# Optimization experiments

Hardware: AMD Instinct MI355X
Metric: run time of the kernel (lower is better)

Reference implementation:

```python
import jax, jax.numpy as jnp
import numpy as np

B, S, W = 32, 128, 20
WV, CV = 50000, 128
WD, CE = 300, 50
KS = (2, 3, 4, 5)
NF = 64
TOTF = NF * len(KS)
CF = 300
H = 512
L = 9
LP = L + 2
START, END = L, L + 1
NEG = -10000.0


def setup_inputs():
    key = jax.random.key(0)
    ks = jax.random.split(key, 40)
    def nrm(i, shape, scale=0.1):
        return jax.random.normal(ks[i], shape, dtype=jnp.float32) * scale
    inp = {}
    inp['token_ids'] = jax.random.randint(ks[0], (B, S), 0, WV)
    inp['char_ids'] = jax.random.randint(ks[1], (B, S, W), 0, CV)
    lens = jnp.sort(jax.random.randint(ks[2], (B,), S // 2, S + 1))[::-1]
    inp['lens'] = lens.astype(jnp.int32)
    inp['labels'] = jax.random.randint(ks[3], (B, S), 0, L)
    inp['word_embed'] = nrm(4, (WV, WD))
    inp['char_embed'] = nrm(5, (CV, CE))
    for j, k in enumerate(KS):
        inp['conv_w%d' % k] = nrm(6 + j, (k, CE, NF))
        inp['conv_b%d' % k] = nrm(10 + j, (NF,))
    inp['ff_w'] = nrm(14, (CF, TOTF))
    inp['ff_b'] = nrm(15, (CF,))
    inp['wgate_w'] = nrm(16, (WD, WD))
    inp['cgate_w'] = nrm(17, (CF, CF))
    inp['gate_w'] = nrm(18, (WD, WD))
    inp['wih_f'] = nrm(19, (4 * H, WD))
    inp['whh_f'] = nrm(20, (4 * H, H))
    inp['b_f'] = nrm(21, (4 * H,))
    inp['wih_b'] = nrm(22, (4 * H, WD))
    inp['whh_b'] = nrm(23, (4 * H, H))
    inp['b_b'] = nrm(24, (4 * H,))
    inp['out_w'] = nrm(25, (L, 2 * H))
    inp['out_b'] = nrm(26, (L,))
    inp['trn'] = nrm(27, (LP, LP))
    return inp


def _char_cnn(char_ids, char_embed, convs):
    x = char_embed[char_ids.reshape(-1, W)]  # [B*S, W, CE]
    feats = []
    for w, b in convs:
        y = jax.lax.conv_general_dilated(x, w, (1,), 'VALID',
                                         dimension_numbers=('NWC', 'WIO', 'NWC')) + b
        feats.append(jnp.max(jax.nn.relu(y), axis=1))  # max over time -> [B*S, NF]
    return jnp.concatenate(feats, axis=1)  # [B*S, TOTF]


def _run_lstm(x, mask, wih, whh, b, reverse):
    # x [B,S,D], mask bool [B,S]; padded steps freeze state and emit zeros (packed-seq semantics)
    xg = jnp.einsum('bsd,gd->bsg', x, wih) + b  # [B,S,4H]
    xg_t = jnp.swapaxes(xg, 0, 1)               # [S,B,4H]
    m_t = jnp.swapaxes(mask, 0, 1)[..., None]   # [S,B,1]
    h0 = jnp.zeros((x.shape[0], H), x.dtype)
    def step(carry, inp):
        h, c = carry
        g_t, m = inp
        g = g_t + h @ whh.T
        i, f, gg, o = jnp.split(g, 4, axis=-1)  # torch gate order i,f,g,o
        cn = jax.nn.sigmoid(f) * c + jax.nn.sigmoid(i) * jnp.tanh(gg)
        hn = jax.nn.sigmoid(o) * jnp.tanh(cn)
        h = jnp.where(m, hn, h)
        c = jnp.where(m, cn, c)
        return (h, c), jnp.where(m, hn, 0.0)
    _, out = jax.lax.scan(step, (h0, h0), (xg_t, m_t), reverse=reverse)
    return jnp.swapaxes(out, 0, 1)  # [B,S,H]


def _crf_norm(logits, mask, trn):
    # logits [B,S,LP]; trn[i,j] = score(prev=j -> next=i)
    alpha = logits[:, 0] + trn[:, START][None, :]
    lt = jnp.swapaxes(logits, 0, 1)[1:]                 # [S-1,B,LP]
    mt = jnp.swapaxes(mask, 0, 1)[1:][..., None]        # [S-1,B,1]
    def step(alpha, inp):
        lg, m = inp
        new = jax.scipy.special.logsumexp(alpha[:, None, :] + trn[None], axis=2) + lg
        return jnp.where(m, new, alpha), None
    alpha, _ = jax.lax.scan(step, alpha, (lt, mt))
    return jax.scipy.special.logsumexp(alpha + trn[END][None, :], axis=1)


def _crf_gold(logits, labels, lens, mask, trn):
    fm = mask.astype(logits.dtype)
    emit = jnp.take_along_axis(logits, labels[..., None], axis=2)[..., 0]
    emit = jnp.sum(emit * fm, axis=1)
    trans = trn[labels[:, 1:], labels[:, :-1]] * fm[:, 1:]
    first = trn[labels[:, 0], START]
    last_lab = jnp.take_along_axis(labels, (lens - 1)[:, None], axis=1)[:, 0]
    return emit + jnp.sum(trans, axis=1) + first + trn[END, last_lab]


def reference(token_ids, char_ids, lens, labels, word_embed, char_embed,
              conv_w2, conv_b2, conv_w3, conv_b3, conv_w4, conv_b4, conv_w5, conv_b5,
              ff_w, ff_b, wgate_w, cgate_w, gate_w,
              wih_f, whh_f, b_f, wih_b, whh_b, b_b, out_w, out_b, trn):
    word_in = word_embed[token_ids]                               # [B,S,WD]
    convs = [(conv_w2, conv_b2), (conv_w3, conv_b3), (conv_w4, conv_b4), (conv_w5, conv_b5)]
    ch = _char_cnn(char_ids, char_embed, convs)                   # [B*S,TOTF]
    char_in = (ch @ ff_w.T + ff_b).reshape(B, S, CF)              # CharCNNFF output
    g = jax.nn.sigmoid(jnp.tanh(word_in @ wgate_w.T + char_in @ cgate_w.T) @ gate_w.T)
    feats = g * word_in + (1.0 - g) * char_in                     # gated fusion (dropout = eval identity)
    mask = jnp.arange(S)[None, :] < lens[:, None]                 # [B,S] bool
    hf = _run_lstm(feats, mask, wih_f, whh_f, b_f, False)
    hb = _run_lstm(feats, mask, wih_b, whh_b, b_b, True)
    lstm_out = jnp.concatenate([hf, hb], axis=-1)                 # [B,S,2H]
    logits = lstm_out @ out_w.T + out_b                           # [B,S,L]
    pads = jnp.full((B, S, 2), NEG, logits.dtype)
    logits = jnp.concatenate([logits, pads], axis=2)              # pad_logits -> [B,S,LP]
    norm = _crf_norm(logits, mask, trn)
    gold = _crf_gold(logits, labels, lens, mask, trn)
    loglik = gold - norm
    return (loglik, logits)
```

## Files before the change

kernel.cpp:

```cpp
#include <hip/hip_runtime.h>

#define NB    32
#define SEQ   128
#define WCH   20
#define CED   50
#define NFLT  64
#define WDIM  300
#define HD    512
#define NWORD 4096
#define LPAD  11
#define NEGV  -10000.0f
#define LSTM_BLOCKS 16

typedef float f32x4 __attribute__((ext_vector_type(4)));
typedef float f32x16 __attribute__((ext_vector_type(16)));
typedef __bf16 bf16x8 __attribute__((ext_vector_type(8)));
typedef unsigned short u16x8 __attribute__((ext_vector_type(8)));
typedef unsigned short u16x4 __attribute__((ext_vector_type(4)));
typedef unsigned long long ull;

static __device__ __forceinline__ unsigned short f2bf(float f) {
  unsigned u = __builtin_bit_cast(unsigned, f);
  u += 0x7fffu + ((u >> 16) & 1u);
  return (unsigned short)(u >> 16);
}
static __device__ __forceinline__ float bf2f(unsigned short s) {
  unsigned u = ((unsigned)s) << 16;
  return __builtin_bit_cast(float, u);
}
static __device__ __forceinline__ float sigf(float x) { return 1.0f / (1.0f + expf(-x)); }

__global__ __launch_bounds__(256) void conv_kernel(
    const int* __restrict__ char_ids, const float* __restrict__ char_embed,
    const float* __restrict__ w2, const float* __restrict__ b2,
    const float* __restrict__ w3, const float* __restrict__ b3,
    const float* __restrict__ w4, const float* __restrict__ b4,
    const float* __restrict__ w5, const float* __restrict__ b5,
    float* __restrict__ ch)
{
  __shared__ __align__(16) float xT[CED][WCH];
  int wi = blockIdx.x;
  int tid = threadIdx.x;
  for (int e = tid; e < WCH * CED; e += 256) {
    int p = e / CED, c = e - p * CED;
    int cid = char_ids[wi * WCH + p];
    xT[c][p] = char_embed[cid * CED + c];
  }
  __syncthreads();
  int w = tid >> 6, f = tid & 63;
  int k = w + 2;
  int P = WCH - k + 1;
  const float* cw = (w == 0) ? w2 : (w == 1) ? w3 : (w == 2) ? w4 : w5;
  const float* cb = (w == 0) ? b2 : (w == 1) ? b3 : (w == 2) ? b4 : b5;
  float acc[19];
  #pragma unroll
  for (int p = 0; p < 19; p++) acc[p] = 0.f;
  for (int c = 0; c < CED; c++) {
    float xr[20];
    const float4* rowp = (const float4*)&xT[c][0];
    #pragma unroll
    for (int q = 0; q < 5; q++) {
      float4 v = rowp[q];
      xr[4*q+0] = v.x; xr[4*q+1] = v.y; xr[4*q+2] = v.z; xr[4*q+3] = v.w;
    }
    #pragma unroll
    for (int dw = 0; dw < 5; dw++) {
      if (dw < k) {
        float wv = cw[(dw * CED + c) * NFLT + f];
        #pragma unroll
        for (int p = 0; p < 19; p++) {
          if (p < P) acc[p] += xr[p + dw] * wv;
        }
      }
    }
  }
  float m = acc[0];
  #pragma unroll
  for (int p = 1; p < 19; p++) if (p < P) m = fmaxf(m, acc[p]);
  ch[wi * 256 + w * 64 + f] = fmaxf(0.f, m + cb[f]);
}

__global__ void gather_word_kernel(const int* __restrict__ token_ids,
                                   const float* __restrict__ word_embed,
                                   float* __restrict__ word_in)
{
  int idx = blockIdx.x * 256 + threadIdx.x;
  if (idx < NWORD * WDIM) {
    int i = idx / WDIM, c = idx - i * WDIM;
    word_in[idx] = word_embed[token_ids[i] * WDIM + c];
  }
}

__global__ __launch_bounds__(256) void gemm_bt_kernel(
    const float* __restrict__ A, const float* __restrict__ Bw,
    const float* __restrict__ bias, const float* __restrict__ Cin,
    float* __restrict__ Cout, unsigned short* __restrict__ Cbf,
    int M, int N, int K, int act, int gridN)
{
  __shared__ __align__(16) unsigned short As[128 * 32];
  __shared__ __align__(16) unsigned short Bs[128 * 32];
  int bid = blockIdx.x;
  int tm = bid / gridN, tn = bid - tm * gridN;
  int m0 = tm * 128, n0 = tn * 128;
  int tid = threadIdx.x;
  int lane = tid & 63, w = tid >> 6;
  int wr = (w >> 1) * 64, wc = (w & 1) * 64;
  f32x4 acc[4][4] = {};
  int fr = lane & 15, fk = (lane >> 4) * 8;

  for (int k0 = 0; k0 < K; k0 += 32) {
    __syncthreads();
    #pragma unroll
    for (int i = 0; i < 4; i++) {
      int idx = tid + i * 256;
      int r = idx >> 3, c4 = idx & 7;
      int kx = k0 + c4 * 4;
      int ra = m0 + r, rb = n0 + r;
      f32x4 av = {0.f,0.f,0.f,0.f}, bv = {0.f,0.f,0.f,0.f};
      if (kx < K) {
        if (ra < M) av = *(const f32x4*)&A[(size_t)ra * K + kx];
        if (rb < N) bv = *(const f32x4*)&Bw[(size_t)rb * K + kx];
      }
      u16x4 ap, bp;
      #pragma unroll
      for (int j = 0; j < 4; j++) { ap[j] = f2bf(av[j]); bp[j] = f2bf(bv[j]); }
      *(u16x4*)&As[r * 32 + c4 * 4] = ap;
      *(u16x4*)&Bs[r * 32 + c4 * 4] = bp;
    }
    __syncthreads();
    bf16x8 a[4], b[4];
    #pragma unroll
    for (int mt = 0; mt < 4; mt++)
      a[mt] = *(const bf16x8*)&As[(wr + mt * 16 + fr) * 32 + fk];
    #pragma unroll
    for (int nt = 0; nt < 4; nt++)
      b[nt] = *(const bf16x8*)&Bs[(wc + nt * 16 + fr) * 32 + fk];
    #pragma unroll
    for (int mt = 0; mt < 4; mt++)
      #pragma unroll
      for (int nt = 0; nt < 4; nt++)
        acc[mt][nt] = __builtin_amdgcn_mfma_f32_16x16x32_bf16(a[mt], b[nt], acc[mt][nt], 0, 0, 0);
  }

  #pragma unroll
  for (int mt = 0; mt < 4; mt++) {
    #pragma unroll
    for (int nt = 0; nt < 4; nt++) {
      #pragma unroll
      for (int j = 0; j < 4; j++) {
        int row = m0 + wr + mt * 16 + (lane >> 4) * 4 + j;
        int col = n0 + wc + nt * 16 + (lane & 15);
        if (row < M && col < N) {
          float v = acc[mt][nt][j];
          if (Cin)  v += Cin[(size_t)row * N + col];
          if (bias) v += bias[col];
          if (act == 1)      v = tanhf(v);
          else if (act == 2) v = sigf(v);
          if (Cbf) Cbf[(size_t)row * N + col] = f2bf(v);
          else     Cout[(size_t)row * N + col] = v;
        }
      }
    }
  }
}

__global__ void feats_kernel(const float* __restrict__ g, const float* __restrict__ word_in,
                             const float* __restrict__ char_in, float* __restrict__ feats,
                             unsigned* __restrict__ flags)
{
  if (blockIdx.x == 0 && threadIdx.x < 32)
    __hip_atomic_store(&flags[threadIdx.x], 0u, __ATOMIC_RELAXED, __HIP_MEMORY_SCOPE_AGENT);
  int idx = blockIdx.x * 256 + threadIdx.x;
  if (idx < NWORD * WDIM) {
    float gg = g[idx];
    feats[idx] = gg * word_in[idx] + (1.f - gg) * char_in[idx];
  }
}

__global__ __launch_bounds__(512, 2) void lstm_kernel(
    const unsigned short* __restrict__ xg_f, const unsigned short* __restrict__ xg_b,
    const float* __restrict__ whh_f, const float* __restrict__ whh_b,
    const int* __restrict__ lens,
    float* __restrict__ lstm_out, unsigned short* __restrict__ h_glob,
    unsigned* __restrict__ flags)
{
  int bid = blockIdx.x;
  int dir = bid >> 3, sl = bid & 7;
  int hs0 = sl << 6;
  int tid = threadIdx.x, lane = tid & 63, w = tid >> 6;
  int g = w & 3, hc = w >> 2;
  int l31 = lane & 31, le = lane >> 5;
  const unsigned short* xg = dir ? xg_b : xg_f;
  const float* whh = dir ? whh_b : whh_f;
  unsigned short* hg = h_glob + dir * (2 * NB * HD);
  unsigned* myflags = flags + dir * 16;

  bf16x8 wf[32];
  {
    const float* src = whh + (size_t)(g * HD + hs0 + hc * 32 + l31) * HD + le * 8;
    #pragma unroll
    for (int kk = 0; kk < 32; kk++) {
      u16x8 tv;
      #pragma unroll
      for (int j = 0; j < 8; j++) tv[j] = f2bf(src[kk * 16 + j]);
      wf[kk] = __builtin_bit_cast(bf16x8, tv);
    }
  }

  __shared__ __align__(16) unsigned short hS[16384];
  __shared__ float Gs[NB][260];

  int b = tid >> 4;
  int u = (tid & 15) << 2;
  int srow = tid >> 4, sq = tid & 15;
  int mylen = lens[b];
  float c4[4] = {0.f,0.f,0.f,0.f}, hp4[4] = {0.f,0.f,0.f,0.f};

  ull xq0, xq1, xq2, xq3;
  {
    int t0 = dir ? (SEQ - 1) : 0;
    const ull* xp = (const ull*)&xg[((size_t)(b * SEQ + t0)) * 2048 + hs0 + u];
    xq0 = xp[0]; xq1 = xp[128]; xq2 = xp[256]; xq3 = xp[384];
  }

  for (int s = 0; s < SEQ; s++) {
    int t = dir ? (SEQ - 1 - s) : s;
    f32x16 acc0 = {}, acc1 = {};

    if (s > 0) {
      if (w == 0) {
        unsigned tgt = (unsigned)s;
        for (;;) {
          unsigned v = (lane < 8)
            ? __hip_atomic_load(&myflags[lane], __ATOMIC_RELAXED, __HIP_MEMORY_SCOPE_AGENT)
            : tgt;
          if (__all(v >= tgt)) break;
          __builtin_amdgcn_s_sleep(1);
        }
      }
      __syncthreads();
      {
        const ull* hq = (const ull*)(hg + (s & 1) * (NB * HD));
        ull v[8];
        #pragma unroll
        for (int i = 0; i < 8; i++)
          v[i] = __hip_atomic_load(hq + srow * 128 + sq * 8 + i, __ATOMIC_RELAXED, __HIP_MEMORY_SCOPE_AGENT);
        int rs = ((srow ^ (sq & 7)) & 31) << 4;
        #pragma unroll
        for (int e2 = 0; e2 < 4; e2++) {
          int kk = 2 * sq + (e2 >> 1), e = e2 & 1;
          uint4 qv;
          qv.x = (unsigned)v[2*e2];     qv.y = (unsigned)(v[2*e2] >> 32);
          qv.z = (unsigned)v[2*e2+1];   qv.w = (unsigned)(v[2*e2+1] >> 32);
          *(uint4*)((char*)hS + (((kk * 2 + e) << 9) + rs)) = qv;
        }
      }
      __syncthreads();
      #pragma unroll
      for (int kk = 0; kk < 32; kk += 2) {
        int rs = ((l31 ^ ((kk >> 1) & 7)) & 31) << 4;
        int a0off = ((kk * 2 + le) << 9) + rs;
        int a1off = ((kk * 2 + 2 + le) << 9) + rs;
        bf16x8 a0 = *(const bf16x8*)((const char*)hS + a0off);
        bf16x8 a1 = *(const bf16x8*)((const char*)hS + a1off);
        acc0 = __builtin_amdgcn_mfma_f32_32x32x16_bf16(a0, wf[kk], acc0, 0, 0, 0);
        acc1 = __builtin_amdgcn_mfma_f32_32x32x16_bf16(a1, wf[kk+1], acc1, 0, 0, 0);
      }
    }

    #pragma unroll
    for (int r = 0; r < 16; r++) {
      int bb = (r & 3) + 8 * (r >> 2) + 4 * le;
      Gs[bb][g * 64 + hc * 32 + l31] = acc0[r] + acc1[r];
    }
    __syncthreads();

    f32x4 gi  = *(const f32x4*)&Gs[b][u];
    f32x4 gfv = *(const f32x4*)&Gs[b][64 + u];
    f32x4 ggv = *(const f32x4*)&Gs[b][128 + u];
    f32x4 gov = *(const f32x4*)&Gs[b][192 + u];
    bool mk = (t < mylen);
    f32x4 outv;
    ull hpk = 0;
    #pragma unroll
    for (int j = 0; j < 4; j++) {
      float xi = bf2f((unsigned short)(xq0 >> (16*j)));
      float xf = bf2f((unsigned short)(xq1 >> (16*j)));
      float xG = bf2f((unsigned short)(xq2 >> (16*j)));
      float xo = bf2f((unsigned short)(xq3 >> (16*j)));
      float iv = sigf(xi + gi[j]);
      float fv = sigf(xf + gfv[j]);
      float Gv = tanhf(xG + ggv[j]);
      float ov = sigf(xo + gov[j]);
      float cn = fv * c4[j] + iv * Gv;
      float hn = ov * tanhf(cn);
      if (mk) c4[j] = cn;
      float hk = mk ? hn : hp4[j];
      hp4[j] = hk;
      outv[j] = mk ? hn : 0.f;
      hpk |= ((ull)f2bf(hk)) << (16*j);
    }
    {
      ull* hd = (ull*)(hg + ((s & 1) ^ 1) * (NB * HD));
      __hip_atomic_store(&hd[(b * HD + hs0 + u) >> 2], hpk, __ATOMIC_RELAXED, __HIP_MEMORY_SCOPE_AGENT);
    }

    __syncthreads();
    if (tid == 0)
      __hip_atomic_store(&myflags[sl], (unsigned)(s + 1), __ATOMIC_RELAXED, __HIP_MEMORY_SCOPE_AGENT);

    size_t obase = ((size_t)(b * SEQ + t)) * 1024 + dir * HD + hs0 + u;
    *(f32x4*)&lstm_out[obase] = outv;
    if (s + 1 < SEQ) {
      int tn = dir ? (SEQ - 2 - s) : (s + 1);
      const ull* xp = (const ull*)&xg[((size_t)(b * SEQ + tn)) * 2048 + hs0 + u];
      xq0 = xp[0]; xq1 = xp[128]; xq2 = xp[256]; xq3 = xp[384];
    }
  }
}

__global__ __launch_bounds__(64) void logits_kernel(
    const float* __restrict__ lstm_out, const float* __restrict__ out_w,
    const float* __restrict__ out_b, float* __restrict__ lg)
{
  int rw = blockIdx.x, j = threadIdx.x;
  const float* row = lstm_out + (size_t)rw * 1024;
  float s[9];
  #pragma unroll
  for (int l = 0; l < 9; l++) s[l] = 0.f;
  for (int e = j; e < 1024; e += 64) {
    float x = row[e];
    #pragma unroll
    for (int l = 0; l < 9; l++) s[l] += x * out_w[l * 1024 + e];
  }
  #pragma unroll
  for (int l = 0; l < 9; l++) {
    #pragma unroll
    for (int off = 32; off > 0; off >>= 1) s[l] += __shfl_xor(s[l], off);
  }
  float v = NEGV;
  if (j < 9) {
    float r = (j==0)?s[0]:(j==1)?s[1]:(j==2)?s[2]:(j==3)?s[3]:(j==4)?s[4]:
              (j==5)?s[5]:(j==6)?s[6]:(j==7)?s[7]:s[8];
    v = r + out_b[j];
  }
  if (j < LPAD) lg[(size_t)rw * LPAD + j] = v;
}

__global__ __launch_bounds__(64) void crf_gold_kernel(
    const float* __restrict__ lg, const int* __restrict__ labels,
    const int* __restrict__ lens, const float* __restrict__ trn, float* __restrict__ gold)
{
  int b = blockIdx.x, j = threadIdx.x;
  int len = lens[b];
  const int* lab = labels + b * SEQ;
  const float* l0 = lg + (size_t)b * SEQ * LPAD;
  float s = 0.f;
  for (int t = j; t < SEQ; t += 64) {
    if (t < len) {
      s += l0[t * LPAD + lab[t]];
      if (t >= 1) s += trn[lab[t] * LPAD + lab[t - 1]];
    }
  }
  #pragma unroll
  for (int off = 32; off > 0; off >>= 1) s += __shfl_xor(s, off);
  if (j == 0) {
    s += trn[lab[0] * LPAD + 9];
    s += trn[10 * LPAD + lab[len - 1]];
    gold[b] = s;
  }
}

__global__ __launch_bounds__(64) void crf_norm_kernel(
    const float* __restrict__ lg, const int* __restrict__ lens,
    const float* __restrict__ trn, const float* __restrict__ gold, float* __restrict__ out_ll)
{
  int b = blockIdx.x, i = threadIdx.x;
  int len = lens[b];
  const float* l0 = lg + (size_t)b * SEQ * LPAD;
  bool act = (i < LPAD);
  float trow[LPAD];
  #pragma unroll
  for (int jj = 0; jj < LPAD; jj++) trow[jj] = act ? trn[i * LPAD + jj] : 0.f;
  float alpha = act ? (l0[i] + trow[9]) : -1e30f;

  for (int t = 1; t < SEQ; t++) {
    float vj[LPAD];
    #pragma unroll
    for (int jj = 0; jj < LPAD; jj++) vj[jj] = __shfl(alpha, jj) + trow[jj];
    float mx = vj[0];
    #pragma unroll
    for (int jj = 1; jj < LPAD; jj++) mx = fmaxf(mx, vj[jj]);
    float sum = 0.f;
    #pragma unroll
    for (int jj = 0; jj < LPAD; jj++) sum += expf(vj[jj] - mx);
    float lgv = act ? l0[t * LPAD + i] : 0.f;
    float nw = mx + logf(sum) + lgv;
    if (act && t < len) alpha = nw;
  }
  float vj[LPAD];
  #pragma unroll
  for (int jj = 0; jj < LPAD; jj++) vj[jj] = __shfl(alpha, jj) + trn[10 * LPAD + jj];
  float mx = vj[0];
  #pragma unroll
  for (int jj = 1; jj < LPAD; jj++) mx = fmaxf(mx, vj[jj]);
  float sum = 0.f;
  #pragma unroll
  for (int jj = 0; jj < LPAD; jj++) sum += expf(vj[jj] - mx);
  if (i == 0) out_ll[b] = gold[b] - (mx + logf(sum));
}

extern "C" void kernel_launch(void* const* d_in, const int* in_sizes, int n_in,
                              void* d_out, int out_size, void* d_ws, size_t ws_size,
                              hipStream_t stream)
{
  (void)in_sizes; (void)n_in; (void)out_size; (void)ws_size;
  const int*   token_ids = (const int*)d_in[0];
  const int*   char_ids  = (const int*)d_in[1];
  const int*   lens      = (const int*)d_in[2];
  const int*   labels    = (const int*)d_in[3];
  const float* word_embed= (const float*)d_in[4];
  const float* char_embed= (const float*)d_in[5];
  const float* w2 = (const float*)d_in[6];  const float* cb2 = (const float*)d_in[7];
  const float* w3 = (const float*)d_in[8];  const float* cb3 = (const float*)d_in[9];
  const float* w4 = (const float*)d_in[10]; const float* cb4 = (const float*)d_in[11];
  const float* w5 = (const float*)d_in[12]; const float* cb5 = (const float*)d_in[13];
  const float* ff_w = (const float*)d_in[14]; const float* ff_b = (const float*)d_in[15];
  const float* wgate_w = (const float*)d_in[16];
  const float* cgate_w = (const float*)d_in[17];
  const float* gate_w  = (const float*)d_in[18];
  const float* wih_f = (const float*)d_in[19]; const float* whh_f = (const float*)d_in[20];
  const float* b_f   = (const float*)d_in[21];
  const float* wih_b = (const float*)d_in[22]; const float* whh_b = (const float*)d_in[23];
  const float* b_b   = (const float*)d_in[24];
  const float* out_w = (const float*)d_in[25]; const float* out_b = (const float*)d_in[26];
  const float* trn   = (const float*)d_in[27];

  char* ws = (char*)d_ws;
  size_t off = 0;
  auto alloc = [&](size_t bytes) { void* p = ws + off; off += (bytes + 255) & ~(size_t)255; return p; };
  float* ch       = (float*)alloc((size_t)NWORD * 256 * 4);
  float* word_in  = (float*)alloc((size_t)NWORD * WDIM * 4);
  float* char_in  = (float*)alloc((size_t)NWORD * WDIM * 4);
  float* t1       = (float*)alloc((size_t)NWORD * WDIM * 4);
  float* gbuf     = (float*)alloc((size_t)NWORD * WDIM * 4);
  float* feats    = (float*)alloc((size_t)NWORD * WDIM * 4);
  unsigned short* xgf = (unsigned short*)alloc((size_t)NWORD * 2048 * 2);
  unsigned short* xgb = (unsigned short*)alloc((size_t)NWORD * 2048 * 2);
  float* lstm_o   = (float*)alloc((size_t)NWORD * 1024 * 4);
  unsigned short* hglob = (unsigned short*)alloc((size_t)2 * 2 * NB * HD * 2);
  float* gold     = (float*)alloc((size_t)NB * 4);
  unsigned* flags = (unsigned*)alloc(256);

  float* outp   = (float*)d_out;
  float* loglik = outp;
  float* logits = outp + NB;

  conv_kernel<<<NWORD, 256, 0, stream>>>(char_ids, char_embed, w2, cb2, w3, cb3, w4, cb4, w5, cb5, ch);
  gather_word_kernel<<<(NWORD * WDIM + 255) / 256, 256, 0, stream>>>(token_ids, word_embed, word_in);
  gemm_bt_kernel<<<32 * 3, 256, 0, stream>>>(ch, ff_w, ff_b, nullptr, char_in, nullptr, NWORD, 300, 256, 0, 3);
  gemm_bt_kernel<<<32 * 3, 256, 0, stream>>>(word_in, wgate_w, nullptr, nullptr, t1, nullptr, NWORD, 300, 300, 0, 3);
  gemm_bt_kernel<<<32 * 3, 256, 0, stream>>>(char_in, cgate_w, nullptr, t1, t1, nullptr, NWORD, 300, 300, 1, 3);
  gemm_bt_kernel<<<32 * 3, 256, 0, stream>>>(t1, gate_w, nullptr, nullptr, gbuf, nullptr, NWORD, 300, 300, 2, 3);
  feats_kernel<<<(NWORD * WDIM + 255) / 256, 256, 0, stream>>>(gbuf, word_in, char_in, feats, flags);
  gemm_bt_kernel<<<32 * 16, 256, 0, stream>>>(feats, wih_f, b_f, nullptr, nullptr, xgf, NWORD, 2048, 300, 0, 16);
  gemm_bt_kernel<<<32 * 16, 256, 0, stream>>>(feats, wih_b, b_b, nullptr, nullptr, xgb, NWORD, 2048, 300, 0, 16);
  {
    void* args[] = { (void*)&xgf, (void*)&xgb, (void*)&whh_f, (void*)&whh_b,
                     (void*)&lens, (void*)&lstm_o, (void*)&hglob, (void*)&flags };
    hipLaunchCooperativeKernel((void*)lstm_kernel, dim3(LSTM_BLOCKS), dim3(512), args, 0, stream);
  }
  logits_kernel<<<NWORD, 64, 0, stream>>>(lstm_o, out_w, out_b, logits);
  crf_gold_kernel<<<NB, 64, 0, stream>>>(logits, labels, lens, trn, gold);
  crf_norm_kernel<<<NB, 64, 0, stream>>>(logits, lens, trn, gold, loglik);
}
```

Measured before the change: 1.283 ms.

## Store pre-LSTM intermediates in bf16 and fuse the gate GEMMs into one kernel

The char-CNN output, word embeddings, gate activations and fused features are now stored in bf16. The dense weights are pre-converted to bf16 by new cvt kernels. The GEMM kernel now loads bf16 directly into LDS with a padded row stride of 40, uses 256x128 tiles with 512 threads, and fuses the word-gate and char-gate GEMMs by concatenating along K with a tanh epilogue. This cuts global memory traffic and per-tile conversion work in the pre-LSTM stage. In exchange it adds six small conversion launches, halves the block count for the N=300 GEMMs, and rounds intermediates like char_in and the gate to bf16.

```diff
diff --git a/kernel.cpp b/kernel.cpp
--- a/kernel.cpp
+++ b/kernel.cpp
@@ -30,13 +30,25 @@
 }
 static __device__ __forceinline__ float sigf(float x) { return 1.0f / (1.0f + expf(-x)); }
 
+__global__ void cvt_kernel(const float* __restrict__ src, unsigned short* __restrict__ dst, int n4)
+{
+  int i = blockIdx.x * 256 + threadIdx.x;
+  if (i < n4) {
+    f32x4 v = *(const f32x4*)&src[i * 4];
+    u16x4 o;
+    #pragma unroll
+    for (int j = 0; j < 4; j++) o[j] = f2bf(v[j]);
+    *(u16x4*)&dst[i * 4] = o;
+  }
+}
+
 __global__ __launch_bounds__(256) void conv_kernel(
     const int* __restrict__ char_ids, const float* __restrict__ char_embed,
     const float* __restrict__ w2, const float* __restrict__ b2,
     const float* __restrict__ w3, const float* __restrict__ b3,
     const float* __restrict__ w4, const float* __restrict__ b4,
     const float* __restrict__ w5, const float* __restrict__ b5,
-    float* __restrict__ ch)
+    unsigned short* __restrict__ ch)
 {
   __shared__ __align__(16) float xT[CED][WCH];
   int wi = blockIdx.x;
@@ -77,64 +89,74 @@
   float m = acc[0];
   #pragma unroll
   for (int p = 1; p < 19; p++) if (p < P) m = fmaxf(m, acc[p]);
-  ch[wi * 256 + w * 64 + f] = fmaxf(0.f, m + cb[f]);
+  ch[wi * 256 + w * 64 + f] = f2bf(fmaxf(0.f, m + cb[f]));
 }
 
 __global__ void gather_word_kernel(const int* __restrict__ token_ids,
                                    const float* __restrict__ word_embed,
-                                   float* __restrict__ word_in)
+                                   unsigned short* __restrict__ word_in)
 {
   int idx = blockIdx.x * 256 + threadIdx.x;
   if (idx < NWORD * WDIM) {
     int i = idx / WDIM, c = idx - i * WDIM;
-    word_in[idx] = word_embed[token_ids[i] * WDIM + c];
-  }
-}
-
-__global__ __launch_bounds__(256) void gemm_bt_kernel(
-    const float* __restrict__ A, const float* __restrict__ Bw,
-    const float* __restrict__ bias, const float* __restrict__ Cin,
-    float* __restrict__ Cout, unsigned short* __restrict__ Cbf,
-    int M, int N, int K, int act, int gridN)
-{
-  __shared__ __align__(16) unsigned short As[128 * 32];
-  __shared__ __align__(16) unsigned short Bs[128 * 32];
+    word_in[idx] = f2bf(word_embed[token_ids[i] * WDIM + c]);
+  }
+}
+
+__global__ __launch_bounds__(512) void gemm2_kernel(
+    const unsigned short* __restrict__ A1, const unsigned short* __restrict__ A2,
+    const unsigned short* __restrict__ B1, const unsigned short* __restrict__ B2,
+    const float* __restrict__ bias, unsigned short* __restrict__ Cbf,
+    int M, int N, int K1, int K2, int act, int gridN)
+{
+  const int Kt = K1 + K2;
+  __shared__ __align__(16) unsigned short As[256 * 40];
+  __shared__ __align__(16) unsigned short Bs[128 * 40];
   int bid = blockIdx.x;
   int tm = bid / gridN, tn = bid - tm * gridN;
-  int m0 = tm * 128, n0 = tn * 128;
+  int m0 = tm * 256, n0 = tn * 128;
   int tid = threadIdx.x;
   int lane = tid & 63, w = tid >> 6;
   int wr = (w >> 1) * 64, wc = (w & 1) * 64;
   f32x4 acc[4][4] = {};
   int fr = lane & 15, fk = (lane >> 4) * 8;
 
-  for (int k0 = 0; k0 < K; k0 += 32) {
+  for (int k0 = 0; k0 < Kt; k0 += 32) {
     __syncthreads();
     #pragma unroll
     for (int i = 0; i < 4; i++) {
-      int idx = tid + i * 256;
-      int r = idx >> 3, c4 = idx & 7;
+      int q = tid + i * 512;
+      int r = q >> 3, c4 = q & 7;
       int kx = k0 + c4 * 4;
-      int ra = m0 + r, rb = n0 + r;
-      f32x4 av = {0.f,0.f,0.f,0.f}, bv = {0.f,0.f,0.f,0.f};
-      if (kx < K) {
-        if (ra < M) av = *(const f32x4*)&A[(size_t)ra * K + kx];
-        if (rb < N) bv = *(const f32x4*)&Bw[(size_t)rb * K + kx];
-      }
-      u16x4 ap, bp;
-      #pragma unroll
-      for (int j = 0; j < 4; j++) { ap[j] = f2bf(av[j]); bp[j] = f2bf(bv[j]); }
-      *(u16x4*)&As[r * 32 + c4 * 4] = ap;
-      *(u16x4*)&Bs[r * 32 + c4 * 4] = bp;
+      int ra = m0 + r;
+      u16x4 v = {0, 0, 0, 0};
+      if (kx < Kt && ra < M) {
+        v = (kx < K1) ? *(const u16x4*)&A1[(size_t)ra * K1 + kx]
+                      : *(const u16x4*)&A2[(size_t)ra * K2 + (kx - K1)];
+      }
+      *(u16x4*)&As[r * 40 + c4 * 4] = v;
+    }
+    #pragma unroll
+    for (int i = 0; i < 2; i++) {
+      int q = tid + i * 512;
+      int r = q >> 3, c4 = q & 7;
+      int kx = k0 + c4 * 4;
+      int rb = n0 + r;
+      u16x4 v = {0, 0, 0, 0};
+      if (kx < Kt && rb < N) {
+        v = (kx < K1) ? *(const u16x4*)&B1[(size_t)rb * K1 + kx]
+                      : *(const u16x4*)&B2[(size_t)rb * K2 + (kx - K1)];
+      }
+      *(u16x4*)&Bs[r * 40 + c4 * 4] = v;
     }
     __syncthreads();
     bf16x8 a[4], b[4];
     #pragma unroll
     for (int mt = 0; mt < 4; mt++)
-      a[mt] = *(const bf16x8*)&As[(wr + mt * 16 + fr) * 32 + fk];
+      a[mt] = *(const bf16x8*)&As[(wr + mt * 16 + fr) * 40 + fk];
     #pragma unroll
     for (int nt = 0; nt < 4; nt++)
-      b[nt] = *(const bf16x8*)&Bs[(wc + nt * 16 + fr) * 32 + fk];
+      b[nt] = *(const bf16x8*)&Bs[(wc + nt * 16 + fr) * 40 + fk];
     #pragma unroll
     for (int mt = 0; mt < 4; mt++)
       #pragma unroll
@@ -152,28 +174,28 @@
         int col = n0 + wc + nt * 16 + (lane & 15);
         if (row < M && col < N) {
           float v = acc[mt][nt][j];
-          if (Cin)  v += Cin[(size_t)row * N + col];
           if (bias) v += bias[col];
           if (act == 1)      v = tanhf(v);
           else if (act == 2) v = sigf(v);
-          if (Cbf) Cbf[(size_t)row * N + col] = f2bf(v);
-          else     Cout[(size_t)row * N + col] = v;
+          Cbf[(size_t)row * N + col] = f2bf(v);
         }
       }
     }
   }
 }
 
-__global__ void feats_kernel(const float* __restrict__ g, const float* __restrict__ word_in,
-                             const float* __restrict__ char_in, float* __restrict__ feats,
+__global__ void feats_kernel(const unsigned short* __restrict__ g,
+                             const unsigned short* __restrict__ word_in,
+                             const unsigned short* __restrict__ char_in,
+                             unsigned short* __restrict__ feats,
                              unsigned* __restrict__ flags)
 {
   if (blockIdx.x == 0 && threadIdx.x < 32)
     __hip_atomic_store(&flags[threadIdx.x], 0u, __ATOMIC_RELAXED, __HIP_MEMORY_SCOPE_AGENT);
   int idx = blockIdx.x * 256 + threadIdx.x;
   if (idx < NWORD * WDIM) {
-    float gg = g[idx];
-    feats[idx] = gg * word_in[idx] + (1.f - gg) * char_in[idx];
+    float gg = bf2f(g[idx]);
+    feats[idx] = f2bf(gg * bf2f(word_in[idx]) + (1.f - gg) * bf2f(char_in[idx]));
   }
 }
 
@@ -439,12 +461,18 @@
   char* ws = (char*)d_ws;
   size_t off = 0;
   auto alloc = [&](size_t bytes) { void* p = ws + off; off += (bytes + 255) & ~(size_t)255; return p; };
-  float* ch       = (float*)alloc((size_t)NWORD * 256 * 4);
-  float* word_in  = (float*)alloc((size_t)NWORD * WDIM * 4);
-  float* char_in  = (float*)alloc((size_t)NWORD * WDIM * 4);
-  float* t1       = (float*)alloc((size_t)NWORD * WDIM * 4);
-  float* gbuf     = (float*)alloc((size_t)NWORD * WDIM * 4);
-  float* feats    = (float*)alloc((size_t)NWORD * WDIM * 4);
+  unsigned short* ch_bf    = (unsigned short*)alloc((size_t)NWORD * 256 * 2);
+  unsigned short* word_bf  = (unsigned short*)alloc((size_t)NWORD * WDIM * 2);
+  unsigned short* char_bf  = (unsigned short*)alloc((size_t)NWORD * WDIM * 2);
+  unsigned short* t1_bf    = (unsigned short*)alloc((size_t)NWORD * WDIM * 2);
+  unsigned short* g_bf     = (unsigned short*)alloc((size_t)NWORD * WDIM * 2);
+  unsigned short* feats_bf = (unsigned short*)alloc((size_t)NWORD * WDIM * 2);
+  unsigned short* ffw_bf   = (unsigned short*)alloc((size_t)300 * 256 * 2);
+  unsigned short* wgw_bf   = (unsigned short*)alloc((size_t)300 * 300 * 2);
+  unsigned short* cgw_bf   = (unsigned short*)alloc((size_t)300 * 300 * 2);
+  unsigned short* gw_bf    = (unsigned short*)alloc((size_t)300 * 300 * 2);
+  unsigned short* wihf_bf  = (unsigned short*)alloc((size_t)2048 * 300 * 2);
+  unsigned short* wihb_bf  = (unsigned short*)alloc((size_t)2048 * 300 * 2);
   unsigned short* xgf = (unsigned short*)alloc((size_t)NWORD * 2048 * 2);
   unsigned short* xgb = (unsigned short*)alloc((size_t)NWORD * 2048 * 2);
   float* lstm_o   = (float*)alloc((size_t)NWORD * 1024 * 4);
@@ -456,15 +484,25 @@
   float* loglik = outp;
   float* logits = outp + NB;
 
-  conv_kernel<<<NWORD, 256, 0, stream>>>(char_ids, char_embed, w2, cb2, w3, cb3, w4, cb4, w5, cb5, ch);
-  gather_word_kernel<<<(NWORD * WDIM + 255) / 256, 256, 0, stream>>>(token_ids, word_embed, word_in);
-  gemm_bt_kernel<<<32 * 3, 256, 0, stream>>>(ch, ff_w, ff_b, nullptr, char_in, nullptr, NWORD, 300, 256, 0, 3);
-  gemm_bt_kernel<<<32 * 3, 256, 0, stream>>>(word_in, wgate_w, nullptr, nullptr, t1, nullptr, NWORD, 300, 300, 0, 3);
-  gemm_bt_kernel<<<32 * 3, 256, 0, stream>>>(char_in, cgate_w, nullptr, t1, t1, nullptr, NWORD, 300, 300, 1, 3);
-  gemm_bt_kernel<<<32 * 3, 256, 0, stream>>>(t1, gate_w, nullptr, nullptr, gbuf, nullptr, NWORD, 300, 300, 2, 3);
-  feats_kernel<<<(NWORD * WDIM + 255) / 256, 256, 0, stream>>>(gbuf, word_in, char_in, feats, flags);
-  gemm_bt_kernel<<<32 * 16, 256, 0, stream>>>(feats, wih_f, b_f, nullptr, nullptr, xgf, NWORD, 2048, 300, 0, 16);
-  gemm_bt_kernel<<<32 * 16, 256, 0, stream>>>(feats, wih_b, b_b, nullptr, nullptr, xgb, NWORD, 2048, 300, 0, 16);
+  conv_kernel<<<NWORD, 256, 0, stream>>>(char_ids, char_embed, w2, cb2, w3, cb3, w4, cb4, w5, cb5, ch_bf);
+  gather_word_kernel<<<(NWORD * WDIM + 255) / 256, 256, 0, stream>>>(token_ids, word_embed, word_bf);
+  cvt_kernel<<<(300*256/4 + 255)/256, 256, 0, stream>>>(ff_w, ffw_bf, 300*256/4);
+  cvt_kernel<<<(300*300/4 + 255)/256, 256, 0, stream>>>(wgate_w, wgw_bf, 300*300/4);
+  cvt_kernel<<<(300*300/4 + 255)/256, 256, 0, stream>>>(cgate_w, cgw_bf, 300*300/4);
+  cvt_kernel<<<(300*300/4 + 255)/256, 256, 0, stream>>>(gate_w, gw_bf, 300*300/4);
+  cvt_kernel<<<(2048*300/4 + 255)/256, 256, 0, stream>>>(wih_f, wihf_bf, 2048*300/4);
+  cvt_kernel<<<(2048*300/4 + 255)/256, 256, 0, stream>>>(wih_b, wihb_bf, 2048*300/4);
+  gemm2_kernel<<<16 * 3, 512, 0, stream>>>(ch_bf, ch_bf, ffw_bf, ffw_bf, ff_b, char_bf,
+                                           NWORD, 300, 256, 0, 0, 3);
+  gemm2_kernel<<<16 * 3, 512, 0, stream>>>(word_bf, char_bf, wgw_bf, cgw_bf, nullptr, t1_bf,
+                                           NWORD, 300, 300, 300, 1, 3);
+  gemm2_kernel<<<16 * 3, 512, 0, stream>>>(t1_bf, t1_bf, gw_bf, gw_bf, nullptr, g_bf,
+                                           NWORD, 300, 300, 0, 2, 3);
+  feats_kernel<<<(NWORD * WDIM + 255) / 256, 256, 0, stream>>>(g_bf, word_bf, char_bf, feats_bf, flags);
+  gemm2_kernel<<<16 * 16, 512, 0, stream>>>(feats_bf, feats_bf, wihf_bf, wihf_bf, b_f, xgf,
+                                            NWORD, 2048, 300, 0, 0, 16);
+  gemm2_kernel<<<16 * 16, 512, 0, stream>>>(feats_bf, feats_bf, wihb_bf, wihb_bf, b_b, xgb,
+                                            NWORD, 2048, 300, 0, 0, 16);
   {
     void* args[] = { (void*)&xgf, (void*)&xgb, (void*)&whh_f, (void*)&whh_b,
                      (void*)&lens, (void*)&lstm_o, (void*)&hglob, (void*)&flags };
```

Result: no change. 1.293 ms (+0.8%).
